# Optimization experiments

Hardware: AMD Instinct MI355X
Metric: run time of the kernel (lower is better)

## Reference

```python
import jax, jax.numpy as jnp
import numpy as np

S_LEN = 4096; HID = 2048
NH = 8; NVH = 16; DK = 128; DV = 128
KEY_DIM = NH * DK; VAL_DIM = NVH * DV
CONV = 4; EPS = 1e-6; GVA = NVH // NH
SCALE = DK ** -0.5


def _short_conv_silu(x, w):
    # causal depthwise conv1d + SiLU: x [S, C], w [C, K]
    K = w.shape[1]
    xp = jnp.pad(x, ((K - 1, 0), (0, 0)))
    y = xp[0:S_LEN] * w[:, 0]
    for j in range(1, K):
        y = y + xp[j:j + S_LEN] * w[:, j]
    return jax.nn.silu(y)


def _l2norm(x):
    return x / jnp.sqrt(jnp.sum(x * x, axis=-1, keepdims=True) + EPS)


def _forward(x, Wq, Wk, Wv, Wa, Wb, Wg, Wo, conv_q, conv_k, conv_v, A_log, dt_bias, w_norm):
    q = _short_conv_silu(x @ Wq.T, conv_q)   # [S, KEY_DIM]
    k = _short_conv_silu(x @ Wk.T, conv_k)
    v = _short_conv_silu(x @ Wv.T, conv_v)   # [S, VAL_DIM]
    q = q.reshape(S_LEN, NH, DK)
    k = k.reshape(S_LEN, NH, DK)
    v = v.reshape(S_LEN, NVH, DV)
    # grouped value attention: each k/q head serves GVA value heads
    q = jnp.repeat(q, GVA, axis=1)           # [S, NVH, DK]
    k = jnp.repeat(k, GVA, axis=1)
    q = _l2norm(q) * SCALE
    k = _l2norm(k)
    beta = jax.nn.sigmoid(x @ Wb.T)          # [S, NVH] delta-rule learning rate
    g = -jnp.exp(A_log) * jax.nn.softplus(x @ Wa.T + dt_bias)  # [S, NVH] log-decay <= 0

    def step(S, inp):
        q_t, k_t, v_t, g_t, b_t = inp        # [H,DK],[H,DK],[H,DV],[H],[H]
        S = S * jnp.exp(g_t)[:, None, None]  # gated decay of memory
        pred = jnp.einsum('hk,hkv->hv', k_t, S)
        delta = (v_t - pred) * b_t[:, None]  # delta-rule update direction
        S = S + jnp.einsum('hk,hv->hkv', k_t, delta)
        o_t = jnp.einsum('hk,hkv->hv', q_t, S)
        return S, o_t

    S0 = jnp.zeros((NVH, DK, DV), x.dtype)
    _, o = jax.lax.scan(step, S0, (q, k, v, g, beta))  # o [S, NVH, DV]

    # FusedRMSNormGated: gate with silu, then RMS-normalize over head_v_dim
    gate = (x @ Wg.T).reshape(S_LEN, NVH, DV)
    og = o * jax.nn.silu(gate)
    og = og * jax.lax.rsqrt(jnp.mean(og * og, axis=-1, keepdims=True) + EPS) * w_norm
    return og.reshape(S_LEN, VAL_DIM) @ Wo.T  # [S, HID]


def setup_inputs() -> dict:
    key = jax.random.key(0)
    ks = jax.random.split(key, 16)
    def lin(k, out_dim, in_dim):
        return jax.random.normal(k, (out_dim, in_dim), jnp.float32) * (in_dim ** -0.5)
    dt = jnp.exp(jax.random.uniform(ks[12], (NVH,)) * (np.log(0.1) - np.log(0.001)) + np.log(0.001))
    dt = jnp.maximum(dt, 1e-4)
    return {
        "x": jax.random.normal(ks[0], (S_LEN, HID), jnp.float32),
        "Wq": lin(ks[1], KEY_DIM, HID),
        "Wk": lin(ks[2], KEY_DIM, HID),
        "Wv": lin(ks[3], VAL_DIM, HID),
        "Wa": lin(ks[4], NVH, HID),
        "Wb": lin(ks[5], NVH, HID),
        "Wg": lin(ks[6], VAL_DIM, HID),
        "Wo": lin(ks[7], HID, VAL_DIM),
        "conv_q": jax.random.normal(ks[8], (KEY_DIM, CONV), jnp.float32) * 0.2,
        "conv_k": jax.random.normal(ks[9], (KEY_DIM, CONV), jnp.float32) * 0.2,
        "conv_v": jax.random.normal(ks[10], (VAL_DIM, CONV), jnp.float32) * 0.2,
        "A_log": jnp.log(jax.random.uniform(ks[11], (NVH,), minval=1.0, maxval=16.0)),
        "dt_bias": dt + jnp.log(-jnp.expm1(-dt)),
        "w_norm": jnp.ones((DV,), jnp.float32),
    }


def reference(x, Wq, Wk, Wv, Wa, Wb, Wg, Wo, conv_q, conv_k, conv_v, A_log, dt_bias, w_norm):
    return _forward(x, Wq, Wk, Wv, Wa, Wb, Wg, Wo, conv_q, conv_k, conv_v, A_log, dt_bias, w_norm)
```

## Files before the change

### kernel.cpp

```cpp
#include <hip/hip_runtime.h>
#include <hip/hip_bf16.h>
#include <math.h>

#define S_LEN 4096
#define HID   2048
#define NH    8
#define NVH   16
#define DK    128
#define DV    128
#define KEY_DIM  (NH*DK)
#define VAL_DIM  (NVH*DV)
#define NPROJ 6144
#define SCALE_Q  0.08838834764831845f
#define CCH 64
#define NCH (S_LEN/CCH)

typedef __attribute__((ext_vector_type(8))) short short8;
typedef __attribute__((ext_vector_type(4))) float f32x4;

__global__ __launch_bounds__(256) void cast_f2b(
    const float* __restrict__ in, __hip_bfloat16* __restrict__ out, int n) {
  int i = (blockIdx.x * 256 + threadIdx.x) * 4;
  if (i >= n) return;
  float4 v = *(const float4*)&in[i];
  union { __hip_bfloat16 b[4]; short4 s; } u;
  u.b[0] = __float2bfloat16(v.x); u.b[1] = __float2bfloat16(v.y);
  u.b[2] = __float2bfloat16(v.z); u.b[3] = __float2bfloat16(v.w);
  *(short4*)&out[i] = u.s;
}

__global__ __launch_bounds__(256) void cast5(
    const float* __restrict__ w0, const float* __restrict__ w1,
    const float* __restrict__ w2, const float* __restrict__ w3,
    const float* __restrict__ w4, __hip_bfloat16* __restrict__ dst) {
  int i = (blockIdx.x * 256 + threadIdx.x) * 4;
  const float* src; int off;
  if      (i <  2097152) { src = w0; off = 0; }
  else if (i <  4194304) { src = w1; off = 2097152; }
  else if (i <  8388608) { src = w2; off = 4194304; }
  else if (i < 12582912) { src = w3; off = 8388608; }
  else                   { src = w4; off = 12582912; }
  float4 v = *(const float4*)&src[i - off];
  union { __hip_bfloat16 b[4]; short4 s; } u;
  u.b[0] = __float2bfloat16(v.x); u.b[1] = __float2bfloat16(v.y);
  u.b[2] = __float2bfloat16(v.z); u.b[3] = __float2bfloat16(v.w);
  *(short4*)&dst[i] = u.s;
}

__device__ __forceinline__ void lds_load16(const __hip_bfloat16* g,
                                           __hip_bfloat16* l) {
  __builtin_amdgcn_global_load_lds(
      (const __attribute__((address_space(1))) unsigned int*)g,
      (__attribute__((address_space(3))) unsigned int*)l, 16, 0, 0);
}

__global__ __launch_bounds__(256) void gemm_bf16_bt(
    const __hip_bfloat16* __restrict__ A, const __hip_bfloat16* __restrict__ B,
    float* __restrict__ C, int M, int N, int K) {
  __shared__ __hip_bfloat16 sA[128 * 32];
  __shared__ __hip_bfloat16 sB[128 * 32];
  const int t = threadIdx.x;
  const int wave = t >> 6, lane = t & 63;
  const int bm = blockIdx.y, bn = blockIdx.x;
  const int wm = (wave & 1) * 64, wn = (wave >> 1) * 64;

  f32x4 zero = {0.f, 0.f, 0.f, 0.f};
  f32x4 acc[4][4];
  #pragma unroll
  for (int i = 0; i < 4; i++)
    #pragma unroll
    for (int j = 0; j < 4; j++) acc[i][j] = zero;

  const int r0 = t >> 2,        c0 = (t & 3) * 8;
  const int r1 = (256 + t) >> 2, c1 = ((256 + t) & 3) * 8;
  const __hip_bfloat16* gA0 = A + (size_t)(bm * 128 + r0) * K + c0;
  const __hip_bfloat16* gA1 = A + (size_t)(bm * 128 + r1) * K + c1;
  const __hip_bfloat16* gB0 = B + (size_t)(bn * 128 + r0) * K + c0;
  const __hip_bfloat16* gB1 = B + (size_t)(bn * 128 + r1) * K + c1;
  __hip_bfloat16* lA0 = sA + (size_t)(wave * 64) * 8;
  __hip_bfloat16* lA1 = sA + (size_t)(256 + wave * 64) * 8;
  __hip_bfloat16* lB0 = sB + (size_t)(wave * 64) * 8;
  __hip_bfloat16* lB1 = sB + (size_t)(256 + wave * 64) * 8;

  const int fm = lane & 15, fk = (lane >> 4) * 8;

  for (int k0 = 0; k0 < K; k0 += 32) {
    lds_load16(gA0, lA0); lds_load16(gA1, lA1);
    lds_load16(gB0, lB0); lds_load16(gB1, lB1);
    gA0 += 32; gA1 += 32; gB0 += 32; gB1 += 32;
    __syncthreads();
    short8 a[4], b[4];
    #pragma unroll
    for (int i = 0; i < 4; i++)
      a[i] = *(const short8*)&sA[(size_t)(wm + i * 16 + fm) * 32 + fk];
    #pragma unroll
    for (int j = 0; j < 4; j++)
      b[j] = *(const short8*)&sB[(size_t)(wn + j * 16 + fm) * 32 + fk];
    #pragma unroll
    for (int i = 0; i < 4; i++)
      #pragma unroll
      for (int j = 0; j < 4; j++)
        acc[i][j] = __builtin_amdgcn_mfma_f32_16x16x32_bf16(a[i], b[j], acc[i][j], 0, 0, 0);
    __syncthreads();
  }
  #pragma unroll
  for (int i = 0; i < 4; i++) {
    #pragma unroll
    for (int j = 0; j < 4; j++) {
      int col = bn * 128 + wn + j * 16 + (lane & 15);
      int rw0 = bm * 128 + wm + i * 16 + (lane >> 4) * 4;
      #pragma unroll
      for (int r = 0; r < 4; r++)
        C[(size_t)(rw0 + r) * N + col] = acc[i][j][r];
    }
  }
}

__global__ __launch_bounds__(256) void gemm_bt2(
    const float* __restrict__ A, const float* __restrict__ Ba,
    const float* __restrict__ Bb, float* __restrict__ Ca,
    float* __restrict__ Cb, int K) {
  const float* B = blockIdx.x == 0 ? Ba : Bb;
  float* C       = blockIdx.x == 0 ? Ca : Cb;
  const int N = NVH;
  __shared__ float As[16][68];
  __shared__ float Bs[16][68];
  const int bm = blockIdx.y;
  const int t = threadIdx.x;
  const int tx = t & 15, ty = t >> 4;
  const int lrow = t >> 2;
  const int lk0  = (t & 3) * 4;
  const int arow = bm * 64 + lrow;
  const bool bvalid = lrow < N;

  float acc[4][4];
  #pragma unroll
  for (int i = 0; i < 4; i++)
    #pragma unroll
    for (int j = 0; j < 4; j++) acc[i][j] = 0.f;

  for (int k0 = 0; k0 < K; k0 += 16) {
    float4 av = *(const float4*)&A[(size_t)arow * K + k0 + lk0];
    float4 bv = bvalid ? *(const float4*)&B[(size_t)lrow * K + k0 + lk0]
                       : make_float4(0.f, 0.f, 0.f, 0.f);
    As[lk0+0][lrow] = av.x; As[lk0+1][lrow] = av.y;
    As[lk0+2][lrow] = av.z; As[lk0+3][lrow] = av.w;
    Bs[lk0+0][lrow] = bv.x; Bs[lk0+1][lrow] = bv.y;
    Bs[lk0+2][lrow] = bv.z; Bs[lk0+3][lrow] = bv.w;
    __syncthreads();
    #pragma unroll
    for (int kk = 0; kk < 16; kk++) {
      float4 a = *(const float4*)&As[kk][ty * 4];
      float4 b = *(const float4*)&Bs[kk][tx * 4];
      float ar[4] = {a.x, a.y, a.z, a.w};
      float br[4] = {b.x, b.y, b.z, b.w};
      #pragma unroll
      for (int i = 0; i < 4; i++)
        #pragma unroll
        for (int j = 0; j < 4; j++) acc[i][j] += ar[i] * br[j];
    }
    __syncthreads();
  }
  #pragma unroll
  for (int i = 0; i < 4; i++) {
    int r = bm * 64 + ty * 4 + i;
    #pragma unroll
    for (int j = 0; j < 4; j++) {
      int c = tx * 4 + j;
      if (c < N) C[(size_t)r * N + c] = acc[i][j];
    }
  }
}

__global__ __launch_bounds__(128) void conv_qk_kernel(
    const float* __restrict__ pre, const float* __restrict__ cwq,
    const float* __restrict__ cwk, __hip_bfloat16* __restrict__ qn,
    __hip_bfloat16* __restrict__ kn) {
  const int s = blockIdx.x, y = blockIdx.y, t = threadIdx.x;
  const bool isq = y < 8;
  const int h = isq ? y : y - 8;
  const int ch = h * 128 + t;
  const float* cw = isq ? cwq : cwk;
  const int col = (isq ? 0 : 1024) + ch;
  const float4 w = *(const float4*)&cw[ch * 4];
  const size_t base = (size_t)s * NPROJ + col;
  float v0 = pre[base] * w.w;
  if (s >= 1) v0 += pre[base - NPROJ]     * w.z;
  if (s >= 2) v0 += pre[base - 2*NPROJ]   * w.y;
  if (s >= 3) v0 += pre[base - 3*NPROJ]   * w.x;
  float v = v0 / (1.f + expf(-v0));
  float ss = v * v;
  #pragma unroll
  for (int off = 1; off < 64; off <<= 1) ss += __shfl_xor(ss, off, 64);
  __shared__ float red[2];
  if ((t & 63) == 0) red[t >> 6] = ss;
  __syncthreads();
  const float scale = isq ? SCALE_Q : 1.f;
  float inv = scale / sqrtf(red[0] + red[1] + 1e-6f);
  __hip_bfloat16* out = isq ? qn : kn;
  out[((size_t)s * NH + h) * 128 + t] = __float2bfloat16(v * inv);
}

__global__ __launch_bounds__(256) void conv_v_kernel(
    const float* __restrict__ pre, const float* __restrict__ cw,
    float* __restrict__ out) {
  const int id = blockIdx.x * 256 + threadIdx.x;
  const int s = id >> 11, c = id & 2047;
  const float4 w = *(const float4*)&cw[c * 4];
  const size_t base = (size_t)s * NPROJ + 2048 + c;
  float y = pre[base] * w.w;
  if (s >= 1) y += pre[base - NPROJ]     * w.z;
  if (s >= 2) y += pre[base - 2*NPROJ]   * w.y;
  if (s >= 3) y += pre[base - 3*NPROJ]   * w.x;
  out[id] = y / (1.f + expf(-y));
}

__global__ __launch_bounds__(256) void gb_kernel(
    const float* __restrict__ a_pre, const float* __restrict__ b_pre,
    const float* __restrict__ A_log, const float* __restrict__ dt_bias,
    float* __restrict__ gl, float* __restrict__ bv) {
  const int id = blockIdx.x * 256 + threadIdx.x;
  const int h = id & 15;
  float av = a_pre[id] + dt_bias[h];
  float sp = av > 20.f ? av : log1pf(expf(av));
  gl[id] = -expf(A_log[h]) * sp;
  bv[id] = 1.f / (1.f + expf(-b_pre[id]));
}

__global__ __launch_bounds__(256) void phaseA_kernel(
    const __hip_bfloat16* __restrict__ kn, const float* __restrict__ vc,
    const float* __restrict__ gl, const float* __restrict__ bvv,
    __hip_bfloat16* __restrict__ Wb, __hip_bfloat16* __restrict__ UbT,
    float* __restrict__ Gbuf) {
  const int h = blockIdx.x, c = blockIdx.y, sh = h >> 1;
  const int t = threadIdx.x, lane = t & 63, w = t >> 6;
  const int fm = lane & 15, fq = lane >> 4;
  __shared__ __hip_bfloat16 kch[64][136];
  __shared__ float vch[64][132];
  __shared__ float mm[64][65];
  __shared__ float sol[64][257];
  __shared__ float Gs[64], bet[64], lamB[64];

  {
    const int r = t >> 2, c0 = (t & 3) * 32;
    const __hip_bfloat16* krow = kn + (size_t)(c*64 + r)*KEY_DIM + sh*128 + c0;
    const float* vrow = vc + (size_t)(c*64 + r)*VAL_DIM + h*128 + c0;
    #pragma unroll
    for (int i = 0; i < 4; i++)
      *(short8*)&kch[r][c0 + 8*i] = *(const short8*)&krow[8*i];
    #pragma unroll
    for (int i = 0; i < 8; i++)
      *(float4*)&vch[r][c0 + 4*i] = *(const float4*)&vrow[4*i];
  }
  if (t < 64) {
    float g = gl[(size_t)(c*64 + t)*NVH + h];
    #pragma unroll
    for (int off = 1; off < 64; off <<= 1) {
      float p = __shfl_up(g, off, 64);
      if (t >= off) g += p;
    }
    Gs[t] = g;
    float b = bvv[(size_t)(c*64 + t)*NVH + h];
    bet[t] = b;
    lamB[t] = b * expf(g);
    Gbuf[((size_t)c*NVH + h)*64 + t] = g;
  }
  __syncthreads();

  {
    f32x4 pacc[4];
    #pragma unroll
    for (int lt = 0; lt < 4; lt++) pacc[lt] = (f32x4){0.f,0.f,0.f,0.f};
    #pragma unroll
    for (int k4 = 0; k4 < 4; k4++) {
      short8 aK = *(const short8*)&kch[16*w + fm][k4*32 + fq*8];
      #pragma unroll
      for (int lt = 0; lt < 4; lt++) {
        short8 bK = *(const short8*)&kch[16*lt + fm][k4*32 + fq*8];
        pacc[lt] = __builtin_amdgcn_mfma_f32_16x16x32_bf16(aK, bK, pacc[lt], 0, 0, 0);
      }
    }
    #pragma unroll
    for (int lt = 0; lt < 4; lt++)
      #pragma unroll
      for (int r2 = 0; r2 < 4; r2++) {
        const int j = 16*w + fq*4 + r2, l = 16*lt + fm;
        mm[j][l] = (l < j) ? bet[j] * expf(Gs[j] - Gs[l]) * pacc[lt][r2] : 0.f;
      }
  }
  __syncthreads();

  {
    const bool isW = t < 128;
    const int col = t & 127;
    for (int j = 0; j < 64; j++) {
      float s0 = isW ? lamB[j] * __bfloat162float(kch[j][col]) : bet[j] * vch[j][col];
      float s1 = 0.f;
      int l = 0;
      for (; l + 1 < j; l += 2) {
        s0 = fmaf(-mm[j][l],   sol[l][t],   s0);
        s1 = fmaf(-mm[j][l+1], sol[l+1][t], s1);
      }
      if (l < j) s0 = fmaf(-mm[j][l], sol[l][t], s0);
      sol[j][t] = s0 + s1;
    }
  }
  if (t < 128) {
    const size_t base = ((size_t)c*NVH + h) * 64 * 128;
    for (int j = 0; j < 64; j++)
      Wb[base + j*128 + t] = __float2bfloat16(sol[j][t]);
  } else {
    const int n = t - 128;
    const size_t ub = (((size_t)c*NVH + h) * 128 + n) * 64;
    for (int j0 = 0; j0 < 64; j0 += 4) {
      union { unsigned long long u; __hip_bfloat16 b[4]; } p;
      #pragma unroll
      for (int i = 0; i < 4; i++) p.b[i] = __float2bfloat16(sol[j0+i][t]);
      *(unsigned long long*)&UbT[ub + j0] = p.u;
    }
  }
}

__device__ __forceinline__ void bar_lgkm() {
  asm volatile("s_waitcnt lgkmcnt(0)" ::: "memory");
  __builtin_amdgcn_s_barrier();
  asm volatile("" ::: "memory");
}

__global__ __launch_bounds__(512, 2) void phaseB_kernel(
    const __hip_bfloat16* __restrict__ qn, const __hip_bfloat16* __restrict__ kn,
    const __hip_bfloat16* __restrict__ Wb, const __hip_bfloat16* __restrict__ UbT,
    const float* __restrict__ Gbuf,
    __hip_bfloat16* __restrict__ Db, float* __restrict__ obuf) {
  const int bid = blockIdx.x;
  const int h = (bid & 7) | ((bid >> 4) << 3);
  const int vt = (bid >> 3) & 1;
  const int sh = h >> 1;
  const int t = threadIdx.x, lane = t & 63, w = t >> 6;
  const int fm = lane & 15, fq = lane >> 4;
  const int jt = w >> 1;
  const int nh = w & 1;
  const int dt = w >> 1;

  __shared__ __hip_bfloat16 S16T[64][136];
  __shared__ __hip_bfloat16 kT[2][128][72];
  __shared__ __hip_bfloat16 dT[64][72];
  __shared__ float Gs[64];

  const int kj = (t & 15) * 4, kd = (t >> 4) * 4;
  const int j0 = 16*jt + fq*4;

  f32x4 Sacc[2][2];
  #pragma unroll
  for (int ti = 0; ti < 2; ti++)
    #pragma unroll
    for (int i = 0; i < 2; i++) Sacc[ti][i] = (f32x4){0.f,0.f,0.f,0.f};
  for (int i = t; i < 64*136/2; i += 512) ((unsigned int*)S16T)[i] = 0;

  ushort4 krg[4];
  short8 Qnext[4], Qcur[4];
  short8 Wnext[4], Wcur[4];
  unsigned long long Unext[2], Ucur[2];
  float gl64;

  auto prefetch = [&](int c) {
    const int cb = (c*NVH + h) * 64;
    const __hip_bfloat16* qbase = qn + (size_t)(c*64 + 16*jt + fm)*KEY_DIM + sh*128 + fq*8;
    #pragma unroll
    for (int k4 = 0; k4 < 4; k4++)
      Qnext[k4] = *(const short8*)&qbase[k4*32];
    #pragma unroll
    for (int jj = 0; jj < 4; jj++)
      krg[jj] = *(const ushort4*)&kn[(size_t)(c*64 + kj + jj)*KEY_DIM + sh*128 + kd];
    #pragma unroll
    for (int k4 = 0; k4 < 4; k4++)
      Wnext[k4] = *(const short8*)&Wb[(size_t)(cb + 16*jt + fm)*128 + k4*32 + fq*8];
    #pragma unroll
    for (int i = 0; i < 2; i++) {
      const int tj = 2*nh + i;
      Unext[i] = *(const unsigned long long*)
          &UbT[(((size_t)c*NVH + h)*128 + vt*64 + 16*tj + fm)*64 + j0];
    }
    if (t < 64) gl64 = Gbuf[(size_t)cb + t];
  };

  auto stage = [&](int buf) {
    if (t < 64) Gs[t] = gl64;
    union { ushort4 v[4]; unsigned short u[16]; } kk;
    #pragma unroll
    for (int jj = 0; jj < 4; jj++) kk.v[jj] = krg[jj];
    #pragma unroll
    for (int dd = 0; dd < 4; dd++) {
      union { unsigned short u[4]; unsigned long long q; } p;
      #pragma unroll
      for (int jj = 0; jj < 4; jj++) p.u[jj] = kk.u[jj*4 + dd];
      *(unsigned long long*)&kT[buf][kd + dd][kj] = p.q;
    }
  };

  prefetch(0);
  #pragma unroll
  for (int k4 = 0; k4 < 4; k4++) { Qcur[k4] = Qnext[k4]; Wcur[k4] = Wnext[k4]; }
  #pragma unroll
  for (int i = 0; i < 2; i++) Ucur[i] = Unext[i];
  bar_lgkm();
  stage(0);
  bar_lgkm();

  for (int c = 0; c < NCH; c++) {
    prefetch(c + 1 < NCH ? c + 1 : 0);

    f32x4 aX[2], aO[2];
    #pragma unroll
    for (int i = 0; i < 2; i++) {
      aX[i] = (f32x4){0.f,0.f,0.f,0.f};
      aO[i] = (f32x4){0.f,0.f,0.f,0.f};
    }
    __builtin_amdgcn_s_setprio(1);
    #pragma unroll
    for (int k4 = 0; k4 < 4; k4++) {
      #pragma unroll
      for (int i = 0; i < 2; i++) {
        const int tj = 2*nh + i;
        short8 b = *(const short8*)&S16T[16*tj + fm][k4*32 + fq*8];
        aX[i] = __builtin_amdgcn_mfma_f32_16x16x32_bf16(Wcur[k4], b, aX[i], 0, 0, 0);
        aO[i] = __builtin_amdgcn_mfma_f32_16x16x32_bf16(Qcur[k4], b, aO[i], 0, 0, 0);
      }
    }
    __builtin_amdgcn_s_setprio(0);
    const int cb = (c*NVH + h) * 64;
    const float gC = Gs[63];
    float er[4], os[4];
    #pragma unroll
    for (int r2 = 0; r2 < 4; r2++) {
      const float gj = Gs[j0 + r2];
      os[r2] = expf(gj);
      er[r2] = expf(gC - gj);
    }
    #pragma unroll
    for (int i = 0; i < 2; i++) {
      const int tj = 2*nh + i;
      const int n = 16*tj + fm;
      union { unsigned long long u; __hip_bfloat16 b[4]; } u4;
      u4.u = Ucur[i];
      union { __hip_bfloat16 b[4]; unsigned long long u; } pd;
      #pragma unroll
      for (int r2 = 0; r2 < 4; r2++) {
        const int j = j0 + r2;
        float d = __bfloat162float(u4.b[r2]) - aX[i][r2];
        Db[(size_t)(cb + j)*128 + vt*64 + n] = __float2bfloat16(d);
        pd.b[r2] = __float2bfloat16(d * er[r2]);
        obuf[((size_t)(c*64 + j)*NVH + h)*128 + vt*64 + n] = aO[i][r2] * os[r2];
      }
      *(unsigned long long*)&dT[n][j0] = pd.u;
    }
    const float lamC = expf(gC);
    #pragma unroll
    for (int ti = 0; ti < 2; ti++)
      #pragma unroll
      for (int i = 0; i < 2; i++)
        #pragma unroll
        for (int r2 = 0; r2 < 4; r2++) Sacc[ti][i][r2] *= lamC;
    bar_lgkm();
    __builtin_amdgcn_s_setprio(1);
    #pragma unroll
    for (int ti = 0; ti < 2; ti++) {
      const int m0 = 32*dt + 16*ti;
      #pragma unroll
      for (int kk0 = 0; kk0 < 64; kk0 += 32) {
        short8 aK = *(const short8*)&kT[c & 1][m0 + fm][kk0 + fq*8];
        #pragma unroll
        for (int i = 0; i < 2; i++) {
          const int tj = 2*nh + i;
          short8 bD = *(const short8*)&dT[16*tj + fm][kk0 + fq*8];
          Sacc[ti][i] = __builtin_amdgcn_mfma_f32_16x16x32_bf16(aK, bD, Sacc[ti][i], 0, 0, 0);
        }
      }
    }
    __builtin_amdgcn_s_setprio(0);
    #pragma unroll
    for (int ti = 0; ti < 2; ti++) {
      const int dk0 = 32*dt + 16*ti + fq*4;
      #pragma unroll
      for (int i = 0; i < 2; i++) {
        const int tj = 2*nh + i;
        const int n = 16*tj + fm;
        union { __hip_bfloat16 b[4]; unsigned long long u; } ps;
        #pragma unroll
        for (int r2 = 0; r2 < 4; r2++) ps.b[r2] = __float2bfloat16(Sacc[ti][i][r2]);
        *(unsigned long long*)&S16T[n][dk0] = ps.u;
      }
    }
    stage((c + 1) & 1);
    #pragma unroll
    for (int k4 = 0; k4 < 4; k4++) { Qcur[k4] = Qnext[k4]; Wcur[k4] = Wnext[k4]; }
    #pragma unroll
    for (int i = 0; i < 2; i++) Ucur[i] = Unext[i];
    bar_lgkm();
  }
}

__global__ __launch_bounds__(256) void phaseC_kernel(
    const __hip_bfloat16* __restrict__ qn, const __hip_bfloat16* __restrict__ kn,
    const float* __restrict__ Gbuf, const __hip_bfloat16* __restrict__ Db,
    float* __restrict__ obuf) {
  const int h = blockIdx.x, c = blockIdx.y, sh = h >> 1;
  const int t = threadIdx.x, lane = t & 63, w = t >> 6;
  const int fm = lane & 15, fq = lane >> 4;
  __shared__ __hip_bfloat16 qch[64][136];
  __shared__ __hip_bfloat16 kch[64][136];
  __shared__ __hip_bfloat16 dchT[128][72];
  __shared__ __hip_bfloat16 Pbf[64][72];
  __shared__ float Gs[64];

  {
    const int r = t >> 2, c0 = (t & 3) * 32;
    const __hip_bfloat16* qrow = qn + (size_t)(c*64 + r)*KEY_DIM + sh*128 + c0;
    const __hip_bfloat16* krow = kn + (size_t)(c*64 + r)*KEY_DIM + sh*128 + c0;
    #pragma unroll
    for (int i = 0; i < 4; i++) {
      *(short8*)&qch[r][c0 + 8*i] = *(const short8*)&qrow[8*i];
      *(short8*)&kch[r][c0 + 8*i] = *(const short8*)&krow[8*i];
    }
    const __hip_bfloat16* drow = Db + ((size_t)c*NVH + h)*64*128 + (size_t)r*128 + c0;
    #pragma unroll
    for (int i = 0; i < 4; i++) {
      union { short8 s; unsigned short u[8]; } dv;
      dv.s = *(const short8*)&drow[8*i];
      #pragma unroll
      for (int e = 0; e < 8; e++)
        *(unsigned short*)&dchT[c0 + 8*i + e][r] = dv.u[e];
    }
  }
  if (t < 64) Gs[t] = Gbuf[((size_t)c*NVH + h)*64 + t];
  __syncthreads();

  {
    f32x4 pacc[4];
    #pragma unroll
    for (int lt = 0; lt < 4; lt++) pacc[lt] = (f32x4){0.f,0.f,0.f,0.f};
    #pragma unroll
    for (int k4 = 0; k4 < 4; k4++) {
      short8 aQ = *(const short8*)&qch[16*w + fm][k4*32 + fq*8];
      #pragma unroll
      for (int lt = 0; lt < 4; lt++) {
        short8 bK = *(const short8*)&kch[16*lt + fm][k4*32 + fq*8];
        pacc[lt] = __builtin_amdgcn_mfma_f32_16x16x32_bf16(aQ, bK, pacc[lt], 0, 0, 0);
      }
    }
    #pragma unroll
    for (int lt = 0; lt < 4; lt++)
      #pragma unroll
      for (int r2 = 0; r2 < 4; r2++) {
        const int j = 16*w + fq*4 + r2, l = 16*lt + fm;
        float v = (l <= j) ? expf(Gs[j] - Gs[l]) * pacc[lt][r2] : 0.f;
        Pbf[j][l] = __float2bfloat16(v);
      }
  }

  {
    f32x4 oacc[8];
    #pragma unroll
    for (int nt = 0; nt < 8; nt++) oacc[nt] = (f32x4){0.f,0.f,0.f,0.f};
    #pragma unroll
    for (int ks = 0; ks < 2; ks++) {
      short8 aP = *(const short8*)&Pbf[16*w + fm][ks*32 + fq*8];
      #pragma unroll
      for (int nt = 0; nt < 8; nt++) {
        short8 bD = *(const short8*)&dchT[16*nt + fm][ks*32 + fq*8];
        oacc[nt] = __builtin_amdgcn_mfma_f32_16x16x32_bf16(aP, bD, oacc[nt], 0, 0, 0);
      }
    }
    #pragma unroll
    for (int nt = 0; nt < 8; nt++)
      #pragma unroll
      for (int r2 = 0; r2 < 4; r2++) {
        const int j = 16*w + fq*4 + r2, n = 16*nt + fm;
        float* p = &obuf[((size_t)(c*64 + j)*NVH + h)*128 + n];
        *p += oacc[nt][r2];
      }
  }
}

__global__ __launch_bounds__(128) void norm_kernel(
    const float* __restrict__ o, const float* __restrict__ pre,
    const float* __restrict__ w_norm, __hip_bfloat16* __restrict__ og) {
  const int s = blockIdx.x, h = blockIdx.y, t = threadIdx.x;
  const size_t idx = (size_t)s * VAL_DIM + h * 128 + t;
  const size_t gidx = (size_t)s * NPROJ + 4096 + h * 128 + t;
  float gt = pre[gidx];
  float val = o[idx] * (gt / (1.f + expf(-gt)));
  float ss = val * val;
  #pragma unroll
  for (int off = 1; off < 64; off <<= 1) ss += __shfl_xor(ss, off, 64);
  __shared__ float red[2];
  if ((t & 63) == 0) red[t >> 6] = ss;
  __syncthreads();
  float ms = (red[0] + red[1]) * (1.f / 128.f);
  og[idx] = __float2bfloat16(val * (1.f / sqrtf(ms + 1e-6f)) * w_norm[t]);
}

extern "C" void kernel_launch(void* const* d_in, const int* in_sizes, int n_in,
                              void* d_out, int out_size, void* d_ws, size_t ws_size,
                              hipStream_t stream) {
  const float* x       = (const float*)d_in[0];
  const float* Wq      = (const float*)d_in[1];
  const float* Wk      = (const float*)d_in[2];
  const float* Wv      = (const float*)d_in[3];
  const float* Wa      = (const float*)d_in[4];
  const float* Wb_     = (const float*)d_in[5];
  const float* Wg      = (const float*)d_in[6];
  const float* Wo      = (const float*)d_in[7];
  const float* conv_q  = (const float*)d_in[8];
  const float* conv_k  = (const float*)d_in[9];
  const float* conv_v  = (const float*)d_in[10];
  const float* A_log   = (const float*)d_in[11];
  const float* dt_bias = (const float*)d_in[12];
  const float* w_norm  = (const float*)d_in[13];
  float* out = (float*)d_out;

  float* W = (float*)d_ws;
  float* pre   = W;
  __hip_bfloat16* qn = (__hip_bfloat16*)(W + 25165824);
  __hip_bfloat16* kn = (__hip_bfloat16*)(W + 27262976);
  float* vcb   = W + 29360128;
  float* a_pre = W + 37748736;
  float* b_pre = a_pre + 65536;
  float* glb   = b_pre + 65536;
  float* beta  = glb + 65536;
  float* Gbuf  = beta + 65536;
  __hip_bfloat16* xb  = (__hip_bfloat16*)(W + 38076416);
  __hip_bfloat16* wts = xb + 8388608;
  __hip_bfloat16* wo  = wts + 12582912;
  __hip_bfloat16* Wbb = (__hip_bfloat16*)(W + 50659328);
  __hip_bfloat16* UbT = (__hip_bfloat16*)(W + 38076416);
  __hip_bfloat16* Db  = (__hip_bfloat16*)(W + 38076416 + 4194304);
  __hip_bfloat16* ogb = Db;
  float* obuf = vcb;

  cast_f2b<<<(S_LEN*HID)/1024, 256, 0, stream>>>(x, xb, S_LEN*HID);
  cast5<<<16777216/1024, 256, 0, stream>>>(Wq, Wk, Wv, Wg, Wo, wts);
  gemm_bt2<<<dim3(2, S_LEN/64), 256, 0, stream>>>(x, Wa, Wb_, a_pre, b_pre, HID);
  gemm_bf16_bt<<<dim3(NPROJ/128, S_LEN/128), 256, 0, stream>>>(xb, wts, pre, S_LEN, NPROJ, HID);
  conv_qk_kernel<<<dim3(S_LEN, 16), 128, 0, stream>>>(pre, conv_q, conv_k, qn, kn);
  conv_v_kernel<<<(S_LEN*VAL_DIM)/256, 256, 0, stream>>>(pre, conv_v, vcb);
  gb_kernel<<<(S_LEN*NVH)/256, 256, 0, stream>>>(a_pre, b_pre, A_log, dt_bias, glb, beta);
  phaseA_kernel<<<dim3(NVH, NCH), 256, 0, stream>>>(kn, vcb, glb, beta, Wbb, UbT, Gbuf);
  phaseB_kernel<<<2*NVH, 512, 0, stream>>>(qn, kn, Wbb, UbT, Gbuf, Db, obuf);
  phaseC_kernel<<<dim3(NVH, NCH), 256, 0, stream>>>(qn, kn, Gbuf, Db, obuf);
  norm_kernel<<<dim3(S_LEN, NVH), 128, 0, stream>>>(obuf, pre, w_norm, ogb);
  gemm_bf16_bt<<<dim3(HID/128, S_LEN/128), 256, 0, stream>>>(ogb, wo, out, S_LEN, HID, VAL_DIM);
}
```

Measured before the change: 1.000 ms.

## Precompute per-chunk affine state transition in phaseA, shrink serial scan, drop phaseC

The chunked delta-rule is reformulated so phaseA, which runs in parallel over chunks, precomputes per-chunk transition matrices (-K^T W and K^T U with decay), a modified query (e^G q - P W) and the intra-chunk output (P U). The serial phaseB scan then only applies S_new = lam*S + B - A S and o += q2 S, with no per-step delta computation, k transpose staging or Db writes. phaseC is removed entirely. In exchange phaseA does more MFMA work, uses about 150KB of LDS and writes larger 128x128 bf16 matrices per chunk, which adds memory traffic and may reduce bf16 accuracy.

```diff
diff --git a/kernel.cpp b/kernel.cpp
--- a/kernel.cpp
+++ b/kernel.cpp
@@ -228,18 +228,26 @@
 }
 
 __global__ __launch_bounds__(256) void phaseA_kernel(
-    const __hip_bfloat16* __restrict__ kn, const float* __restrict__ vc,
+    const __hip_bfloat16* __restrict__ qn, const __hip_bfloat16* __restrict__ kn,
+    float* __restrict__ vc,
     const float* __restrict__ gl, const float* __restrict__ bvv,
-    __hip_bfloat16* __restrict__ Wb, __hip_bfloat16* __restrict__ UbT,
-    float* __restrict__ Gbuf) {
+    __hip_bfloat16* __restrict__ amNeg, __hip_bfloat16* __restrict__ Bmo,
+    __hip_bfloat16* __restrict__ q2, float* __restrict__ lam) {
   const int h = blockIdx.x, c = blockIdx.y, sh = h >> 1;
   const int t = threadIdx.x, lane = t & 63, w = t >> 6;
   const int fm = lane & 15, fq = lane >> 4;
-  __shared__ __hip_bfloat16 kch[64][136];
-  __shared__ float vch[64][132];
-  __shared__ float mm[64][65];
-  __shared__ float sol[64][257];
-  __shared__ float Gs[64], bet[64], lamB[64];
+
+  __shared__ char smem[153088];
+  __hip_bfloat16* kch = (__hip_bfloat16*)(smem);
+  __hip_bfloat16* kTe = (__hip_bfloat16*)(smem + 17408);
+  float* vch = (float*)(smem + 35840);
+  float* mm  = (float*)(smem + 69632);
+  float* sol = (float*)(smem + 86272);
+  float* Gs  = (float*)(smem + 152064);
+  float* bet = Gs + 64; float* lamB = bet + 64; float* er = lamB + 64;
+  __hip_bfloat16* WT = (__hip_bfloat16*)(smem + 35840);
+  __hip_bfloat16* UT = (__hip_bfloat16*)(smem + 54272);
+  __hip_bfloat16* Pl = (__hip_bfloat16*)(smem + 86272);
 
   {
     const int r = t >> 2, c0 = (t & 3) * 32;
@@ -247,10 +255,10 @@
     const float* vrow = vc + (size_t)(c*64 + r)*VAL_DIM + h*128 + c0;
     #pragma unroll
     for (int i = 0; i < 4; i++)
-      *(short8*)&kch[r][c0 + 8*i] = *(const short8*)&krow[8*i];
+      *(short8*)&kch[r*136 + c0 + 8*i] = *(const short8*)&krow[8*i];
     #pragma unroll
     for (int i = 0; i < 8; i++)
-      *(float4*)&vch[r][c0 + 4*i] = *(const float4*)&vrow[4*i];
+      *(float4*)&vch[r*132 + c0 + 4*i] = *(const float4*)&vrow[4*i];
   }
   if (t < 64) {
     float g = gl[(size_t)(c*64 + t)*NVH + h];
@@ -260,10 +268,12 @@
       if (t >= off) g += p;
     }
     Gs[t] = g;
+    float gC = __shfl(g, 63, 64);
+    er[t] = expf(gC - g);
     float b = bvv[(size_t)(c*64 + t)*NVH + h];
     bet[t] = b;
     lamB[t] = b * expf(g);
-    Gbuf[((size_t)c*NVH + h)*64 + t] = g;
+    if (t == 0) lam[c*NVH + h] = expf(gC);
   }
   __syncthreads();
 
@@ -273,10 +283,10 @@
     for (int lt = 0; lt < 4; lt++) pacc[lt] = (f32x4){0.f,0.f,0.f,0.f};
     #pragma unroll
     for (int k4 = 0; k4 < 4; k4++) {
-      short8 aK = *(const short8*)&kch[16*w + fm][k4*32 + fq*8];
+      short8 aK = *(const short8*)&kch[(16*w + fm)*136 + k4*32 + fq*8];
       #pragma unroll
       for (int lt = 0; lt < 4; lt++) {
-        short8 bK = *(const short8*)&kch[16*lt + fm][k4*32 + fq*8];
+        short8 bK = *(const short8*)&kch[(16*lt + fm)*136 + k4*32 + fq*8];
         pacc[lt] = __builtin_amdgcn_mfma_f32_16x16x32_bf16(aK, bK, pacc[lt], 0, 0, 0);
       }
     }
@@ -285,8 +295,17 @@
       #pragma unroll
       for (int r2 = 0; r2 < 4; r2++) {
         const int j = 16*w + fq*4 + r2, l = 16*lt + fm;
-        mm[j][l] = (l < j) ? bet[j] * expf(Gs[j] - Gs[l]) * pacc[lt][r2] : 0.f;
-      }
+        mm[j*65 + l] = (l < j) ? bet[j] * expf(Gs[j] - Gs[l]) * pacc[lt][r2] : 0.f;
+      }
+  }
+  {
+    const int dk = t >> 1, jh = (t & 1) * 32;
+    for (int j = jh; j < jh + 32; j += 2) {
+      union { __hip_bfloat16 b[2]; unsigned u; } p;
+      p.b[0] = __float2bfloat16(er[j]   * __bfloat162float(kch[j*136 + dk]));
+      p.b[1] = __float2bfloat16(er[j+1] * __bfloat162float(kch[(j+1)*136 + dk]));
+      *(unsigned*)&kTe[dk*72 + j] = p.u;
+    }
   }
   __syncthreads();
 
@@ -294,29 +313,111 @@
     const bool isW = t < 128;
     const int col = t & 127;
     for (int j = 0; j < 64; j++) {
-      float s0 = isW ? lamB[j] * __bfloat162float(kch[j][col]) : bet[j] * vch[j][col];
+      float s0 = isW ? lamB[j] * __bfloat162float(kch[j*136 + col])
+                     : bet[j] * vch[j*132 + col];
       float s1 = 0.f;
       int l = 0;
       for (; l + 1 < j; l += 2) {
-        s0 = fmaf(-mm[j][l],   sol[l][t],   s0);
-        s1 = fmaf(-mm[j][l+1], sol[l+1][t], s1);
-      }
-      if (l < j) s0 = fmaf(-mm[j][l], sol[l][t], s0);
-      sol[j][t] = s0 + s1;
-    }
-  }
-  if (t < 128) {
-    const size_t base = ((size_t)c*NVH + h) * 64 * 128;
-    for (int j = 0; j < 64; j++)
-      Wb[base + j*128 + t] = __float2bfloat16(sol[j][t]);
-  } else {
-    const int n = t - 128;
-    const size_t ub = (((size_t)c*NVH + h) * 128 + n) * 64;
-    for (int j0 = 0; j0 < 64; j0 += 4) {
-      union { unsigned long long u; __hip_bfloat16 b[4]; } p;
-      #pragma unroll
-      for (int i = 0; i < 4; i++) p.b[i] = __float2bfloat16(sol[j0+i][t]);
-      *(unsigned long long*)&UbT[ub + j0] = p.u;
+        s0 = fmaf(-mm[j*65 + l],     sol[l*257 + t],     s0);
+        s1 = fmaf(-mm[j*65 + l + 1], sol[(l+1)*257 + t], s1);
+      }
+      if (l < j) s0 = fmaf(-mm[j*65 + l], sol[l*257 + t], s0);
+      sol[j*257 + t] = s0 + s1;
+    }
+  }
+  __syncthreads();
+
+  f32x4 pP[4];
+  #pragma unroll
+  for (int lt = 0; lt < 4; lt++) pP[lt] = (f32x4){0.f,0.f,0.f,0.f};
+  {
+    short8 aQ[4];
+    #pragma unroll
+    for (int k4 = 0; k4 < 4; k4++)
+      aQ[k4] = *(const short8*)&qn[((size_t)(c*64 + 16*w + fm)*NH + sh)*128 + k4*32 + fq*8];
+    #pragma unroll
+    for (int k4 = 0; k4 < 4; k4++)
+      #pragma unroll
+      for (int lt = 0; lt < 4; lt++) {
+        short8 bK = *(const short8*)&kch[(16*lt + fm)*136 + k4*32 + fq*8];
+        pP[lt] = __builtin_amdgcn_mfma_f32_16x16x32_bf16(aQ[k4], bK, pP[lt], 0, 0, 0);
+      }
+  }
+  {
+    const int colv = t & 127;
+    const int base = (t < 128) ? 0 : 128;
+    __hip_bfloat16* Tdst = (t < 128) ? WT : UT;
+    for (int j = 0; j < 64; j += 2) {
+      union { __hip_bfloat16 b[2]; unsigned u; } p;
+      p.b[0] = __float2bfloat16(sol[j*257 + base + colv]);
+      p.b[1] = __float2bfloat16(sol[(j+1)*257 + base + colv]);
+      *(unsigned*)&Tdst[colv*72 + j] = p.u;
+    }
+  }
+  __syncthreads();
+
+  #pragma unroll
+  for (int lt = 0; lt < 4; lt++)
+    #pragma unroll
+    for (int r2 = 0; r2 < 4; r2++) {
+      const int j = 16*w + fq*4 + r2, l = 16*lt + fm;
+      float v = (l <= j) ? expf(Gs[j] - Gs[l]) * pP[lt][r2] : 0.f;
+      Pl[j*72 + l] = __float2bfloat16(v);
+    }
+  __syncthreads();
+
+  const size_t gb = ((size_t)c*NVH + h) * 128;
+  #pragma unroll
+  for (int ti = 0; ti < 2; ti++) {
+    const int m0 = 32*w + 16*ti;
+    short8 aK[2];
+    #pragma unroll
+    for (int ks = 0; ks < 2; ks++)
+      aK[ks] = *(const short8*)&kTe[(m0 + fm)*72 + ks*32 + fq*8];
+    #pragma unroll
+    for (int nt = 0; nt < 8; nt++) {
+      f32x4 aA = (f32x4){0.f,0.f,0.f,0.f}, aB = (f32x4){0.f,0.f,0.f,0.f};
+      #pragma unroll
+      for (int ks = 0; ks < 2; ks++) {
+        short8 bW = *(const short8*)&WT[(16*nt + fm)*72 + ks*32 + fq*8];
+        short8 bU = *(const short8*)&UT[(16*nt + fm)*72 + ks*32 + fq*8];
+        aA = __builtin_amdgcn_mfma_f32_16x16x32_bf16(aK[ks], bW, aA, 0, 0, 0);
+        aB = __builtin_amdgcn_mfma_f32_16x16x32_bf16(aK[ks], bU, aB, 0, 0, 0);
+      }
+      #pragma unroll
+      for (int r2 = 0; r2 < 4; r2++) {
+        const int row = m0 + fq*4 + r2, col = 16*nt + fm;
+        const size_t idx = (gb + row)*128 + col;
+        amNeg[idx] = __float2bfloat16(-aA[r2]);
+        Bmo[idx]   = __float2bfloat16(aB[r2]);
+      }
+    }
+  }
+  {
+    float eg[4];
+    #pragma unroll
+    for (int r2 = 0; r2 < 4; r2++) eg[r2] = expf(Gs[16*w + fq*4 + r2]);
+    short8 aP[2];
+    #pragma unroll
+    for (int ks = 0; ks < 2; ks++)
+      aP[ks] = *(const short8*)&Pl[(16*w + fm)*72 + ks*32 + fq*8];
+    #pragma unroll
+    for (int nt = 0; nt < 8; nt++) {
+      f32x4 aR = (f32x4){0.f,0.f,0.f,0.f}, aO = (f32x4){0.f,0.f,0.f,0.f};
+      #pragma unroll
+      for (int ks = 0; ks < 2; ks++) {
+        short8 bW = *(const short8*)&WT[(16*nt + fm)*72 + ks*32 + fq*8];
+        short8 bU = *(const short8*)&UT[(16*nt + fm)*72 + ks*32 + fq*8];
+        aR = __builtin_amdgcn_mfma_f32_16x16x32_bf16(aP[ks], bW, aR, 0, 0, 0);
+        aO = __builtin_amdgcn_mfma_f32_16x16x32_bf16(aP[ks], bU, aO, 0, 0, 0);
+      }
+      #pragma unroll
+      for (int r2 = 0; r2 < 4; r2++) {
+        const int j = 16*w + fq*4 + r2, dk = 16*nt + fm;
+        float qv = __bfloat162float(qn[((size_t)(c*64 + j)*NH + sh)*128 + dk]);
+        q2[(((size_t)c*NVH + h)*64 + j)*128 + dk] = __float2bfloat16(eg[r2]*qv - aR[r2]);
+        vc[((size_t)(c*64 + j)*NVH + h)*128 + dk] = aO[r2];
+      }
     }
   }
 }
@@ -328,257 +429,141 @@
 }
 
 __global__ __launch_bounds__(512, 2) void phaseB_kernel(
-    const __hip_bfloat16* __restrict__ qn, const __hip_bfloat16* __restrict__ kn,
-    const __hip_bfloat16* __restrict__ Wb, const __hip_bfloat16* __restrict__ UbT,
-    const float* __restrict__ Gbuf,
-    __hip_bfloat16* __restrict__ Db, float* __restrict__ obuf) {
+    const __hip_bfloat16* __restrict__ q2, const __hip_bfloat16* __restrict__ amNeg,
+    const __hip_bfloat16* __restrict__ Bmo, const float* __restrict__ lam,
+    float* __restrict__ obuf) {
   const int bid = blockIdx.x;
   const int h = (bid & 7) | ((bid >> 4) << 3);
   const int vt = (bid >> 3) & 1;
-  const int sh = h >> 1;
   const int t = threadIdx.x, lane = t & 63, w = t >> 6;
   const int fm = lane & 15, fq = lane >> 4;
-  const int jt = w >> 1;
-  const int nh = w & 1;
-  const int dt = w >> 1;
+  const int jt = w >> 1, nh = w & 1, dt = w >> 1;
 
   __shared__ __hip_bfloat16 S16T[64][136];
-  __shared__ __hip_bfloat16 kT[2][128][72];
-  __shared__ __hip_bfloat16 dT[64][72];
-  __shared__ float Gs[64];
-
-  const int kj = (t & 15) * 4, kd = (t >> 4) * 4;
-  const int j0 = 16*jt + fq*4;
+  for (int i = t; i < 64*136/2; i += 512) ((unsigned*)S16T)[i] = 0;
 
   f32x4 Sacc[2][2];
   #pragma unroll
   for (int ti = 0; ti < 2; ti++)
     #pragma unroll
     for (int i = 0; i < 2; i++) Sacc[ti][i] = (f32x4){0.f,0.f,0.f,0.f};
-  for (int i = t; i < 64*136/2; i += 512) ((unsigned int*)S16T)[i] = 0;
-
-  ushort4 krg[4];
-  short8 Qnext[4], Qcur[4];
-  short8 Wnext[4], Wcur[4];
-  unsigned long long Unext[2], Ucur[2];
-  float gl64;
+
+  short8 Qn[4], Qc[4];
+  short8 An[2][4], Ac[2][4];
+  __hip_bfloat16 Bn[2][2][4], Bc[2][2][4];
+  float On[2][4], Oc[2][4];
+  float lamn, lamc;
 
   auto prefetch = [&](int c) {
-    const int cb = (c*NVH + h) * 64;
-    const __hip_bfloat16* qbase = qn + (size_t)(c*64 + 16*jt + fm)*KEY_DIM + sh*128 + fq*8;
+    const size_t hb = (size_t)c*NVH + h;
     #pragma unroll
     for (int k4 = 0; k4 < 4; k4++)
-      Qnext[k4] = *(const short8*)&qbase[k4*32];
-    #pragma unroll
-    for (int jj = 0; jj < 4; jj++)
-      krg[jj] = *(const ushort4*)&kn[(size_t)(c*64 + kj + jj)*KEY_DIM + sh*128 + kd];
-    #pragma unroll
-    for (int k4 = 0; k4 < 4; k4++)
-      Wnext[k4] = *(const short8*)&Wb[(size_t)(cb + 16*jt + fm)*128 + k4*32 + fq*8];
-    #pragma unroll
-    for (int i = 0; i < 2; i++) {
-      const int tj = 2*nh + i;
-      Unext[i] = *(const unsigned long long*)
-          &UbT[(((size_t)c*NVH + h)*128 + vt*64 + 16*tj + fm)*64 + j0];
-    }
-    if (t < 64) gl64 = Gbuf[(size_t)cb + t];
+      Qn[k4] = *(const short8*)&q2[(hb*64 + 16*jt + fm)*128 + k4*32 + fq*8];
+    #pragma unroll
+    for (int ti = 0; ti < 2; ti++)
+      #pragma unroll
+      for (int k4 = 0; k4 < 4; k4++)
+        An[ti][k4] = *(const short8*)&amNeg[(hb*128 + 32*dt + 16*ti + fm)*128 + k4*32 + fq*8];
+    #pragma unroll
+    for (int ti = 0; ti < 2; ti++)
+      #pragma unroll
+      for (int i = 0; i < 2; i++)
+        #pragma unroll
+        for (int r2 = 0; r2 < 4; r2++)
+          Bn[ti][i][r2] = Bmo[(hb*128 + 32*dt + 16*ti + fq*4 + r2)*128 + vt*64 + 16*(2*nh+i) + fm];
+    #pragma unroll
+    for (int i = 0; i < 2; i++)
+      #pragma unroll
+      for (int r2 = 0; r2 < 4; r2++)
+        On[i][r2] = obuf[((size_t)(c*64 + 16*jt + fq*4 + r2)*NVH + h)*128 + vt*64 + 16*(2*nh+i) + fm];
+    lamn = lam[c*NVH + h];
   };
 
-  auto stage = [&](int buf) {
-    if (t < 64) Gs[t] = gl64;
-    union { ushort4 v[4]; unsigned short u[16]; } kk;
-    #pragma unroll
-    for (int jj = 0; jj < 4; jj++) kk.v[jj] = krg[jj];
-    #pragma unroll
-    for (int dd = 0; dd < 4; dd++) {
-      union { unsigned short u[4]; unsigned long long q; } p;
-      #pragma unroll
-      for (int jj = 0; jj < 4; jj++) p.u[jj] = kk.u[jj*4 + dd];
-      *(unsigned long long*)&kT[buf][kd + dd][kj] = p.q;
-    }
+  auto pull = [&]() {
+    #pragma unroll
+    for (int k4 = 0; k4 < 4; k4++) Qc[k4] = Qn[k4];
+    #pragma unroll
+    for (int ti = 0; ti < 2; ti++)
+      #pragma unroll
+      for (int k4 = 0; k4 < 4; k4++) Ac[ti][k4] = An[ti][k4];
+    #pragma unroll
+    for (int ti = 0; ti < 2; ti++)
+      #pragma unroll
+      for (int i = 0; i < 2; i++)
+        #pragma unroll
+        for (int r2 = 0; r2 < 4; r2++) Bc[ti][i][r2] = Bn[ti][i][r2];
+    #pragma unroll
+    for (int i = 0; i < 2; i++)
+      #pragma unroll
+      for (int r2 = 0; r2 < 4; r2++) Oc[i][r2] = On[i][r2];
+    lamc = lamn;
   };
 
   prefetch(0);
-  #pragma unroll
-  for (int k4 = 0; k4 < 4; k4++) { Qcur[k4] = Qnext[k4]; Wcur[k4] = Wnext[k4]; }
-  #pragma unroll
-  for (int i = 0; i < 2; i++) Ucur[i] = Unext[i];
-  bar_lgkm();
-  stage(0);
+  pull();
   bar_lgkm();
 
   for (int c = 0; c < NCH; c++) {
     prefetch(c + 1 < NCH ? c + 1 : 0);
 
-    f32x4 aX[2], aO[2];
-    #pragma unroll
-    for (int i = 0; i < 2; i++) {
-      aX[i] = (f32x4){0.f,0.f,0.f,0.f};
-      aO[i] = (f32x4){0.f,0.f,0.f,0.f};
-    }
+    short8 sB[2][4];
+    #pragma unroll
+    for (int i = 0; i < 2; i++)
+      #pragma unroll
+      for (int k4 = 0; k4 < 4; k4++)
+        sB[i][k4] = *(const short8*)&S16T[16*(2*nh+i) + fm][k4*32 + fq*8];
+
     __builtin_amdgcn_s_setprio(1);
-    #pragma unroll
-    for (int k4 = 0; k4 < 4; k4++) {
-      #pragma unroll
-      for (int i = 0; i < 2; i++) {
-        const int tj = 2*nh + i;
-        short8 b = *(const short8*)&S16T[16*tj + fm][k4*32 + fq*8];
-        aX[i] = __builtin_amdgcn_mfma_f32_16x16x32_bf16(Wcur[k4], b, aX[i], 0, 0, 0);
-        aO[i] = __builtin_amdgcn_mfma_f32_16x16x32_bf16(Qcur[k4], b, aO[i], 0, 0, 0);
-      }
-    }
-    __builtin_amdgcn_s_setprio(0);
-    const int cb = (c*NVH + h) * 64;
-    const float gC = Gs[63];
-    float er[4], os[4];
-    #pragma unroll
-    for (int r2 = 0; r2 < 4; r2++) {
-      const float gj = Gs[j0 + r2];
-      os[r2] = expf(gj);
-      er[r2] = expf(gC - gj);
-    }
-    #pragma unroll
-    for (int i = 0; i < 2; i++) {
-      const int tj = 2*nh + i;
-      const int n = 16*tj + fm;
-      union { unsigned long long u; __hip_bfloat16 b[4]; } u4;
-      u4.u = Ucur[i];
-      union { __hip_bfloat16 b[4]; unsigned long long u; } pd;
-      #pragma unroll
-      for (int r2 = 0; r2 < 4; r2++) {
-        const int j = j0 + r2;
-        float d = __bfloat162float(u4.b[r2]) - aX[i][r2];
-        Db[(size_t)(cb + j)*128 + vt*64 + n] = __float2bfloat16(d);
-        pd.b[r2] = __float2bfloat16(d * er[r2]);
-        obuf[((size_t)(c*64 + j)*NVH + h)*128 + vt*64 + n] = aO[i][r2] * os[r2];
-      }
-      *(unsigned long long*)&dT[n][j0] = pd.u;
-    }
-    const float lamC = expf(gC);
+    f32x4 aO[2];
+    #pragma unroll
+    for (int i = 0; i < 2; i++) aO[i] = (f32x4){0.f,0.f,0.f,0.f};
+    #pragma unroll
+    for (int k4 = 0; k4 < 4; k4++)
+      #pragma unroll
+      for (int i = 0; i < 2; i++)
+        aO[i] = __builtin_amdgcn_mfma_f32_16x16x32_bf16(Qc[k4], sB[i][k4], aO[i], 0, 0, 0);
+    f32x4 acc[2][2];
     #pragma unroll
     for (int ti = 0; ti < 2; ti++)
       #pragma unroll
       for (int i = 0; i < 2; i++)
         #pragma unroll
-        for (int r2 = 0; r2 < 4; r2++) Sacc[ti][i][r2] *= lamC;
+        for (int r2 = 0; r2 < 4; r2++)
+          acc[ti][i][r2] = lamc * Sacc[ti][i][r2] + __bfloat162float(Bc[ti][i][r2]);
+    #pragma unroll
+    for (int k4 = 0; k4 < 4; k4++)
+      #pragma unroll
+      for (int ti = 0; ti < 2; ti++)
+        #pragma unroll
+        for (int i = 0; i < 2; i++)
+          acc[ti][i] = __builtin_amdgcn_mfma_f32_16x16x32_bf16(Ac[ti][k4], sB[i][k4], acc[ti][i], 0, 0, 0);
+    __builtin_amdgcn_s_setprio(0);
+
+    #pragma unroll
+    for (int i = 0; i < 2; i++)
+      #pragma unroll
+      for (int r2 = 0; r2 < 4; r2++)
+        obuf[((size_t)(c*64 + 16*jt + fq*4 + r2)*NVH + h)*128 + vt*64 + 16*(2*nh+i) + fm]
+            = Oc[i][r2] + aO[i][r2];
+    #pragma unroll
+    for (int ti = 0; ti < 2; ti++)
+      #pragma unroll
+      for (int i = 0; i < 2; i++) Sacc[ti][i] = acc[ti][i];
+
     bar_lgkm();
-    __builtin_amdgcn_s_setprio(1);
-    #pragma unroll
-    for (int ti = 0; ti < 2; ti++) {
-      const int m0 = 32*dt + 16*ti;
-      #pragma unroll
-      for (int kk0 = 0; kk0 < 64; kk0 += 32) {
-        short8 aK = *(const short8*)&kT[c & 1][m0 + fm][kk0 + fq*8];
-        #pragma unroll
-        for (int i = 0; i < 2; i++) {
-          const int tj = 2*nh + i;
-          short8 bD = *(const short8*)&dT[16*tj + fm][kk0 + fq*8];
-          Sacc[ti][i] = __builtin_amdgcn_mfma_f32_16x16x32_bf16(aK, bD, Sacc[ti][i], 0, 0, 0);
-        }
-      }
-    }
-    __builtin_amdgcn_s_setprio(0);
     #pragma unroll
     for (int ti = 0; ti < 2; ti++) {
       const int dk0 = 32*dt + 16*ti + fq*4;
       #pragma unroll
       for (int i = 0; i < 2; i++) {
-        const int tj = 2*nh + i;
-        const int n = 16*tj + fm;
         union { __hip_bfloat16 b[4]; unsigned long long u; } ps;
         #pragma unroll
         for (int r2 = 0; r2 < 4; r2++) ps.b[r2] = __float2bfloat16(Sacc[ti][i][r2]);
-        *(unsigned long long*)&S16T[n][dk0] = ps.u;
-      }
-    }
-    stage((c + 1) & 1);
-    #pragma unroll
-    for (int k4 = 0; k4 < 4; k4++) { Qcur[k4] = Qnext[k4]; Wcur[k4] = Wnext[k4]; }
-    #pragma unroll
-    for (int i = 0; i < 2; i++) Ucur[i] = Unext[i];
+        *(unsigned long long*)&S16T[16*(2*nh+i) + fm][dk0] = ps.u;
+      }
+    }
+    pull();
     bar_lgkm();
-  }
-}
-
-__global__ __launch_bounds__(256) void phaseC_kernel(
-    const __hip_bfloat16* __restrict__ qn, const __hip_bfloat16* __restrict__ kn,
-    const float* __restrict__ Gbuf, const __hip_bfloat16* __restrict__ Db,
-    float* __restrict__ obuf) {
-  const int h = blockIdx.x, c = blockIdx.y, sh = h >> 1;
-  const int t = threadIdx.x, lane = t & 63, w = t >> 6;
-  const int fm = lane & 15, fq = lane >> 4;
-  __shared__ __hip_bfloat16 qch[64][136];
-  __shared__ __hip_bfloat16 kch[64][136];
-  __shared__ __hip_bfloat16 dchT[128][72];
-  __shared__ __hip_bfloat16 Pbf[64][72];
-  __shared__ float Gs[64];
-
-  {
-    const int r = t >> 2, c0 = (t & 3) * 32;
-    const __hip_bfloat16* qrow = qn + (size_t)(c*64 + r)*KEY_DIM + sh*128 + c0;
-    const __hip_bfloat16* krow = kn + (size_t)(c*64 + r)*KEY_DIM + sh*128 + c0;
-    #pragma unroll
-    for (int i = 0; i < 4; i++) {
-      *(short8*)&qch[r][c0 + 8*i] = *(const short8*)&qrow[8*i];
-      *(short8*)&kch[r][c0 + 8*i] = *(const short8*)&krow[8*i];
-    }
-    const __hip_bfloat16* drow = Db + ((size_t)c*NVH + h)*64*128 + (size_t)r*128 + c0;
-    #pragma unroll
-    for (int i = 0; i < 4; i++) {
-      union { short8 s; unsigned short u[8]; } dv;
-      dv.s = *(const short8*)&drow[8*i];
-      #pragma unroll
-      for (int e = 0; e < 8; e++)
-        *(unsigned short*)&dchT[c0 + 8*i + e][r] = dv.u[e];
-    }
-  }
-  if (t < 64) Gs[t] = Gbuf[((size_t)c*NVH + h)*64 + t];
-  __syncthreads();
-
-  {
-    f32x4 pacc[4];
-    #pragma unroll
-    for (int lt = 0; lt < 4; lt++) pacc[lt] = (f32x4){0.f,0.f,0.f,0.f};
-    #pragma unroll
-    for (int k4 = 0; k4 < 4; k4++) {
-      short8 aQ = *(const short8*)&qch[16*w + fm][k4*32 + fq*8];
-      #pragma unroll
-      for (int lt = 0; lt < 4; lt++) {
-        short8 bK = *(const short8*)&kch[16*lt + fm][k4*32 + fq*8];
-        pacc[lt] = __builtin_amdgcn_mfma_f32_16x16x32_bf16(aQ, bK, pacc[lt], 0, 0, 0);
-      }
-    }
-    #pragma unroll
-    for (int lt = 0; lt < 4; lt++)
-      #pragma unroll
-      for (int r2 = 0; r2 < 4; r2++) {
-        const int j = 16*w + fq*4 + r2, l = 16*lt + fm;
-        float v = (l <= j) ? expf(Gs[j] - Gs[l]) * pacc[lt][r2] : 0.f;
-        Pbf[j][l] = __float2bfloat16(v);
-      }
-  }
-
-  {
-    f32x4 oacc[8];
-    #pragma unroll
-    for (int nt = 0; nt < 8; nt++) oacc[nt] = (f32x4){0.f,0.f,0.f,0.f};
-    #pragma unroll
-    for (int ks = 0; ks < 2; ks++) {
-      short8 aP = *(const short8*)&Pbf[16*w + fm][ks*32 + fq*8];
-      #pragma unroll
-      for (int nt = 0; nt < 8; nt++) {
-        short8 bD = *(const short8*)&dchT[16*nt + fm][ks*32 + fq*8];
-        oacc[nt] = __builtin_amdgcn_mfma_f32_16x16x32_bf16(aP, bD, oacc[nt], 0, 0, 0);
-      }
-    }
-    #pragma unroll
-    for (int nt = 0; nt < 8; nt++)
-      #pragma unroll
-      for (int r2 = 0; r2 < 4; r2++) {
-        const int j = 16*w + fq*4 + r2, n = 16*nt + fm;
-        float* p = &obuf[((size_t)(c*64 + j)*NVH + h)*128 + n];
-        *p += oacc[nt][r2];
-      }
   }
 }
 
@@ -628,14 +613,14 @@
   float* b_pre = a_pre + 65536;
   float* glb   = b_pre + 65536;
   float* beta  = glb + 65536;
-  float* Gbuf  = beta + 65536;
+  float* lam   = W + 38010880;
   __hip_bfloat16* xb  = (__hip_bfloat16*)(W + 38076416);
   __hip_bfloat16* wts = xb + 8388608;
   __hip_bfloat16* wo  = wts + 12582912;
-  __hip_bfloat16* Wbb = (__hip_bfloat16*)(W + 50659328);
-  __hip_bfloat16* UbT = (__hip_bfloat16*)(W + 38076416);
-  __hip_bfloat16* Db  = (__hip_bfloat16*)(W + 38076416 + 4194304);
-  __hip_bfloat16* ogb = Db;
+  __hip_bfloat16* amNeg = (__hip_bfloat16*)(W + 38076416);
+  __hip_bfloat16* Bmo = (__hip_bfloat16*)(W + 50659328);
+  __hip_bfloat16* q2b = (__hip_bfloat16*)(W + 59047936);
+  __hip_bfloat16* ogb = (__hip_bfloat16*)(W + 25165824);
   float* obuf = vcb;
 
   cast_f2b<<<(S_LEN*HID)/1024, 256, 0, stream>>>(x, xb, S_LEN*HID);
@@ -645,9 +630,8 @@
   conv_qk_kernel<<<dim3(S_LEN, 16), 128, 0, stream>>>(pre, conv_q, conv_k, qn, kn);
   conv_v_kernel<<<(S_LEN*VAL_DIM)/256, 256, 0, stream>>>(pre, conv_v, vcb);
   gb_kernel<<<(S_LEN*NVH)/256, 256, 0, stream>>>(a_pre, b_pre, A_log, dt_bias, glb, beta);
-  phaseA_kernel<<<dim3(NVH, NCH), 256, 0, stream>>>(kn, vcb, glb, beta, Wbb, UbT, Gbuf);
-  phaseB_kernel<<<2*NVH, 512, 0, stream>>>(qn, kn, Wbb, UbT, Gbuf, Db, obuf);
-  phaseC_kernel<<<dim3(NVH, NCH), 256, 0, stream>>>(qn, kn, Gbuf, Db, obuf);
+  phaseA_kernel<<<dim3(NVH, NCH), 256, 0, stream>>>(qn, kn, vcb, glb, beta, amNeg, Bmo, q2b, lam);
+  phaseB_kernel<<<2*NVH, 512, 0, stream>>>(q2b, amNeg, Bmo, lam, obuf);
   norm_kernel<<<dim3(S_LEN, NVH), 128, 0, stream>>>(obuf, pre, w_norm, ogb);
   gemm_bf16_bt<<<dim3(HID/128, S_LEN/128), 256, 0, stream>>>(ogb, wo, out, S_LEN, HID, VAL_DIM);
 }
```

After: 984.1 us. No clear change (-1.6%).
